# Kernel tuning notes

Measured on AMD Instinct MI355X. Metric: run time of the kernel, lower is better.

Reference implementation:

```python
import jax, jax.numpy as jnp
import numpy as np

NEG_SLOPE = 0.2
CHUNK = 64  # target-node chunk size to bound the [B,c,N,H,D] intermediate


def layer_norm(x, g, b, eps=1e-5):
    mu = jnp.mean(x, axis=-1, keepdims=True)
    var = jnp.mean((x - mu) ** 2, axis=-1, keepdims=True)
    return (x - mu) / jnp.sqrt(var + eps) * g + b


def gatv2_dense(x, Wl, bl, Wr, br, att, bias):
    """GATv2 (PyG semantics, concat=True) on a fully-connected graph with self-loops.
    x: [B,N,Fin]; att: [H,D]. Returns [B,N,H*D].
    e_ij = att_h . leaky_relu(xl_j + xr_i); softmax over sources j; out_i = sum_j a_ij xl_j.
    """
    B, N, _ = x.shape
    H, D = att.shape
    xl = (x @ Wl + bl).reshape(B, N, H, D)  # source-side (lin_l)
    xr = (x @ Wr + br).reshape(B, N, H, D)  # target-side (lin_r)
    nc = N // CHUNK
    xr_ch = jnp.moveaxis(xr.reshape(B, nc, CHUNK, H, D), 1, 0)  # [nc,B,c,H,D]

    @jax.checkpoint
    def per_chunk(xr_c):  # xr_c: [B,c,H,D]
        z = jax.nn.leaky_relu(xr_c[:, :, None] + xl[:, None], NEG_SLOPE)  # [B,c,N,H,D]
        e = jnp.einsum('bcjhd,hd->bcjh', z, att)
        a = jax.nn.softmax(e, axis=2)  # softmax over sources j
        return jnp.einsum('bcjh,bjhd->bchd', a, xl)

    out = jax.lax.map(per_chunk, xr_ch)  # [nc,B,c,H,D]
    return jnp.moveaxis(out, 0, 1).reshape(B, N, H * D) + bias


def setup_inputs() -> dict:
    key = jax.random.key(0)
    ks = jax.random.split(key, 12)
    B, N, Fin, Hd, H, Do = 4, 2048, 32, 32, 4, 32
    f32 = jnp.float32

    def glorot(k, shape, fan_in):
        return jax.random.normal(k, shape, f32) * (1.0 / np.sqrt(fan_in))

    return {
        'x': jax.random.normal(ks[0], (B, N, Fin), f32),
        'embedding': jax.random.normal(ks[1], (N, Hd), f32),
        # layer 1: in=Fin, heads=H, head dim=Hd
        'Wl1': glorot(ks[2], (Fin, H * Hd), Fin), 'bl1': jnp.zeros((H * Hd,), f32),
        'Wr1': glorot(ks[3], (Fin, H * Hd), Fin), 'br1': jnp.zeros((H * Hd,), f32),
        'att1': glorot(ks[4], (H, Hd), Hd), 'bias1': jnp.zeros((H * Hd,), f32),
        'ln1_g': jnp.ones((H * Hd,), f32), 'ln1_b': jnp.zeros((H * Hd,), f32),
        # layer 2: in=H*Hd, heads=H, head dim=Do
        'Wl2': glorot(ks[5], (H * Hd, H * Do), H * Hd), 'bl2': jnp.zeros((H * Do,), f32),
        'Wr2': glorot(ks[6], (H * Hd, H * Do), H * Hd), 'br2': jnp.zeros((H * Do,), f32),
        'att2': glorot(ks[7], (H, Do), Do), 'bias2': jnp.zeros((H * Do,), f32),
        'ln2_g': jnp.ones((H * Do,), f32), 'ln2_b': jnp.zeros((H * Do,), f32),
    }


def reference(x, embedding, Wl1, bl1, Wr1, br1, att1, bias1, ln1_g, ln1_b,
              Wl2, bl2, Wr2, br2, att2, bias2, ln2_g, ln2_b):
    # AdaptiveAdjacency: cosine-similarity gram matrix. Its values are generically
    # all nonzero, so adj[b].nonzero() yields a fully-connected edge list including
    # self-loops; only the connectivity (dense) is consumed downstream.
    ne = embedding / jnp.linalg.norm(embedding, axis=1, keepdims=True)
    adj = ne @ ne.T  # [N,N]; connectivity only (dense), values unused by GATv2
    del adj

    h = layer_norm(gatv2_dense(x, Wl1, bl1, Wr1, br1, att1, bias1), ln1_g, ln1_b)
    h = jax.nn.relu(h)
    # dropout(p=0.3) is identity in eval mode
    out = layer_norm(gatv2_dense(h, Wl2, bl2, Wr2, br2, att2, bias2), ln2_g, ln2_b)
    return out
```

## Files before the change

kernel.cpp:

```cpp
#include <hip/hip_runtime.h>
#include <math.h>

#define LOG2E 1.4426950408889634f

#if __has_builtin(__builtin_amdgcn_exp2f)
#define EXP2(x) __builtin_amdgcn_exp2f(x)
#else
#define EXP2(x) exp2f(x)
#endif

constexpr int B_ = 4, N_ = 2048, H_ = 4, D_ = 32, HD_ = 128;
constexpr int BH_ = B_ * H_;
constexpr int ROWS_ = BH_ * N_;
constexpr size_t M_ = (size_t)ROWS_ * D_;

typedef float v4f __attribute__((ext_vector_type(4)));
typedef _Float16 h2 __attribute__((ext_vector_type(2)));

static __device__ __forceinline__ h2 habs2(h2 z) {
    unsigned int t = __builtin_bit_cast(unsigned int, z) & 0x7FFF7FFFu;
    return __builtin_bit_cast(h2, t);
}
static __device__ __forceinline__ h2 hadd2u(unsigned int a, unsigned int b) {
    return __builtin_bit_cast(h2, a) + __builtin_bit_cast(h2, b);
}
static __device__ __forceinline__ h2 u2h(unsigned int a) {
    return __builtin_bit_cast(h2, a);
}

__global__ __launch_bounds__(256) void k_linear(
    const float* __restrict__ x,
    const float* __restrict__ Wl, const float* __restrict__ bl,
    const float* __restrict__ Wr, const float* __restrict__ br,
    float* __restrict__ xl, unsigned short* __restrict__ xlh,
    unsigned short* __restrict__ xrh, unsigned int* __restrict__ xlpT, int K)
{
    __shared__ __align__(16) float xs[32 * 128];
    const int tid = threadIdx.x;
    const int r0 = blockIdx.x * 32;
    const float4* src = (const float4*)(x + (size_t)r0 * K);
    float4* dst = (float4*)xs;
    for (int idx = tid; idx < 8 * K; idx += 256) dst[idx] = src[idx];
    __syncthreads();

    const int c  = tid & 127;
    const int rg = tid >> 7;
    float accl[16], accr[16];
    const float blv = bl[c], brv = br[c];
    #pragma unroll
    for (int r = 0; r < 16; r++) { accl[r] = blv; accr[r] = brv; }
    #pragma unroll 8
    for (int k = 0; k < K; k++) {
        const float wl = Wl[k * HD_ + c];
        const float wr = Wr[k * HD_ + c];
        #pragma unroll
        for (int r = 0; r < 16; r++) {
            const float xv = xs[(rg * 16 + r) * K + k];
            accl[r] = fmaf(xv, wl, accl[r]);
            accr[r] = fmaf(xv, wr, accr[r]);
        }
    }
    const int h = c >> 5, d = c & 31;
    #pragma unroll
    for (int r = 0; r < 16; r++) {
        const int row = r0 + rg * 16 + r;
        const int b = row >> 11, n = row & (N_ - 1);
        const size_t o = (((size_t)(b * H_ + h)) * N_ + n) * D_ + d;
        xl[o] = accl[r];
        xlh[o] = __builtin_bit_cast(unsigned short, (_Float16)accl[r]);
        xrh[o] = __builtin_bit_cast(unsigned short, (_Float16)accr[r]);
    }
    #pragma unroll
    for (int r = 0; r < 16; r += 2) {
        const int row = r0 + rg * 16 + r;
        const int b = row >> 11, n = row & (N_ - 1);
        h2 pr;
        pr.x = (_Float16)accl[r];
        pr.y = (_Float16)accl[r + 1];
        const size_t o = (((size_t)(b * H_ + h)) * (N_ / 2) + (n >> 1)) * D_ + d;
        xlpT[o] = __builtin_bit_cast(unsigned int, pr);
    }
}

__global__ __launch_bounds__(256) void k_u(
    const float* __restrict__ xl, const float* __restrict__ att,
    float* __restrict__ u)
{
    const int idx = blockIdx.x * 256 + threadIdx.x;
    const int h = (idx / N_) & (H_ - 1);
    const float4* a4 = (const float4*)(att + h * D_);
    const float4* l4 = (const float4*)(xl + (size_t)idx * D_);
    float su = 0.f;
    #pragma unroll
    for (int q = 0; q < 8; q++) {
        const float4 a = a4[q], lv = l4[q];
        su += a.x * lv.x + a.y * lv.y + a.z * lv.z + a.w * lv.w;
    }
    u[idx] = 0.6f * LOG2E * su;
}

__global__ __launch_bounds__(512) void k_bound(
    const unsigned int* __restrict__ xlh, const unsigned int* __restrict__ xrh,
    const float* __restrict__ u, const float* __restrict__ att,
    float* __restrict__ bound, unsigned int* __restrict__ tch)
{
    __shared__ float redA[16][33];
    __shared__ float redB[16][33];
    __shared__ float clv[32];
    __shared__ float tca[32];
    __shared__ float redu[512];
    const int bh = blockIdx.x, h = bh & (H_ - 1), t = threadIdx.x;

    if (bh < H_ && t < 16) {
        h2 v;
        v.x = (_Float16)(att[bh * D_ + 2 * t]     * (0.4f * LOG2E));
        v.y = (_Float16)(att[bh * D_ + 2 * t + 1] * (0.4f * LOG2E));
        tch[bh * 16 + t] = __builtin_bit_cast(unsigned int, v);
    }
    if (t < 16) {
        _Float16 a = (_Float16)(att[h * D_ + 2 * t]     * (0.4f * LOG2E));
        _Float16 b = (_Float16)(att[h * D_ + 2 * t + 1] * (0.4f * LOG2E));
        tca[2 * t]     = fabsf((float)a);
        tca[2 * t + 1] = fabsf((float)b);
    }
    const unsigned int* xb = xlh + (size_t)bh * N_ * 16;
    const int p = t & 15, rg = t >> 4;
    float m0 = 0.f, m1 = 0.f;
    for (int r = rg; r < N_; r += 32) {
        h2 z = __builtin_bit_cast(h2, xb[r * 16 + p] & 0x7FFF7FFFu);
        m0 = fmaxf(m0, (float)z.x);
        m1 = fmaxf(m1, (float)z.y);
    }
    redA[p][rg] = m0; redB[p][rg] = m1;
    const float* ub = u + (size_t)bh * N_;
    float um = -1e30f;
    for (int r = t; r < N_; r += 512) um = fmaxf(um, ub[r]);
    redu[t] = um;
    __syncthreads();
    if (t < 16) {
        float a = 0.f, b = 0.f;
        for (int g = 0; g < 32; g++) { a = fmaxf(a, redA[t][g]); b = fmaxf(b, redB[t][g]); }
        clv[2 * t] = a; clv[2 * t + 1] = b;
    }
    for (int s = 256; s > 0; s >>= 1) {
        if (t < s) redu[t] = fmaxf(redu[t], redu[t + s]);
        __syncthreads();
    }
    const float umax = redu[0];
    const unsigned int* xrb = xrh + (size_t)bh * N_ * 16;
    for (int r = t; r < N_; r += 512) {
        float s = 0.f;
        #pragma unroll
        for (int k = 0; k < 16; k++) {
            h2 z = __builtin_bit_cast(h2, xrb[r * 16 + k] & 0x7FFF7FFFu);
            s += tca[2 * k] * (clv[2 * k] + (float)z.x)
               + tca[2 * k + 1] * (clv[2 * k + 1] + (float)z.y);
        }
        bound[bh * N_ + r] = umax + s + 0.25f;
    }
}

__global__ __launch_bounds__(256)
__attribute__((amdgpu_waves_per_eu(3, 4)))
void k_attn(
    const unsigned int* __restrict__ xlh,
    const unsigned int* __restrict__ xlpT,
    const unsigned int* __restrict__ xrh,
    const float* __restrict__ u, const float* __restrict__ bound,
    const unsigned int* __restrict__ tch,
    float* __restrict__ P, float* __restrict__ lb, int jlen)
{
    const int tid = threadIdx.x, lane = tid & 63, wid = tid >> 6;
    const int t128 = blockIdx.x & 127, part = blockIdx.x >> 7;
    const int bh = t128 >> 3;
    const int h  = bh & (H_ - 1);
    const int row = bh * N_ + (t128 & 7) * 256 + wid * 64 + lane;

    unsigned int tcs[16];
    #pragma unroll
    for (int k = 0; k < 16; k++)
        tcs[k] = __builtin_amdgcn_readfirstlane(tch[h * 16 + k]);

    unsigned int xrp[16];
    {
        const uint4* s = (const uint4*)(xrh + (size_t)row * 16);
        const uint4 a = s[0], b = s[1], c = s[2], d = s[3];
        xrp[0]=a.x; xrp[1]=a.y; xrp[2]=a.z; xrp[3]=a.w;
        xrp[4]=b.x; xrp[5]=b.y; xrp[6]=b.z; xrp[7]=b.w;
        xrp[8]=c.x; xrp[9]=c.y; xrp[10]=c.z; xrp[11]=c.w;
        xrp[12]=d.x; xrp[13]=d.y; xrp[14]=d.z; xrp[15]=d.w;
    }
    const float negb = -bound[row];

    float l = 0.f;
    float o[32];
    #pragma unroll
    for (int k = 0; k < 32; k++) o[k] = 0.f;

    const unsigned int* xlh_b = xlh + (size_t)bh * N_ * 16;
    const unsigned int* xlt_b = xlpT + (size_t)bh * (N_ / 2) * 32;
    const float* u_b = u + (size_t)bh * N_;

    const int jpb = (part * jlen) >> 1, jpe = jpb + (jlen >> 1);
    for (int jp = jpb; jp < jpe; jp++) {
        const unsigned int* w0 = xlh_b + (size_t)(2 * jp) * 16;
        const unsigned int* w1 = w0 + 16;
        float e0 = u_b[2 * jp]     + negb;
        float f0 = 0.f, e1 = u_b[2 * jp + 1] + negb, f1 = 0.f;
        #pragma unroll
        for (int k = 0; k < 16; k += 2) {
            e0 = __builtin_amdgcn_fdot2(habs2(hadd2u(w0[k],     xrp[k])),     u2h(tcs[k]),     e0, false);
            f0 = __builtin_amdgcn_fdot2(habs2(hadd2u(w0[k + 1], xrp[k + 1])), u2h(tcs[k + 1]), f0, false);
            e1 = __builtin_amdgcn_fdot2(habs2(hadd2u(w1[k],     xrp[k])),     u2h(tcs[k]),     e1, false);
            f1 = __builtin_amdgcn_fdot2(habs2(hadd2u(w1[k + 1], xrp[k + 1])), u2h(tcs[k + 1]), f1, false);
        }
        const float p0 = EXP2(e0 + f0);
        const float p1 = EXP2(e1 + f1);
        const h2 p01 = __builtin_bit_cast(h2, __builtin_amdgcn_cvt_pkrtz(p0, p1));
        h2 ones; ones.x = (_Float16)1.f; ones.y = (_Float16)1.f;
        l = __builtin_amdgcn_fdot2(p01, ones, l, false);
        const unsigned int* vp = xlt_b + (size_t)jp * 32;
        #pragma unroll
        for (int d = 0; d < 32; d++)
            o[d] = __builtin_amdgcn_fdot2(p01, u2h(vp[d]), o[d], false);
    }

    float* Pp = P + (size_t)part * M_ + (size_t)row * D_;
    #pragma unroll
    for (int k = 0; k < 8; k++) {
        v4f w;
        w.x = o[4*k]; w.y = o[4*k+1]; w.z = o[4*k+2]; w.w = o[4*k+3];
        ((v4f*)Pp)[k] = w;
    }
    lb[part * ROWS_ + row] = l;
}

template <int JS>
__global__ __launch_bounds__(64) void k_comb_ln(
    const float* __restrict__ P, const float* __restrict__ lb,
    const float* __restrict__ bias, const float* __restrict__ g,
    const float* __restrict__ bta, float* __restrict__ outp, int do_relu)
{
    const int row = blockIdx.x;
    const int b = row >> 11, n = row & (N_ - 1);
    const int t = threadIdx.x;
    const int c0 = t, c1 = t + 64;
    const int bh0 = b * H_ + (c0 >> 5), bh1 = b * H_ + (c1 >> 5);
    const size_t i0 = ((size_t)bh0 * N_ + n) * D_ + (c0 & 31);
    const size_t i1 = ((size_t)bh1 * N_ + n) * D_ + (c1 & 31);
    float a0 = 0.f, a1 = 0.f, L0 = 0.f, L1 = 0.f;
    #pragma unroll
    for (int s = 0; s < JS; s++) {
        a0 += P[(size_t)s * M_ + i0];
        a1 += P[(size_t)s * M_ + i1];
        L0 += lb[s * ROWS_ + bh0 * N_ + n];
        L1 += lb[s * ROWS_ + bh1 * N_ + n];
    }
    const float x0 = a0 / L0 + bias[c0];
    const float x1 = a1 / L1 + bias[c1];
    float s = x0 + x1;
    #pragma unroll
    for (int w = 1; w < 64; w <<= 1) s += __shfl_xor(s, w);
    const float mu = s * (1.f / 128.f);
    const float d0 = x0 - mu, d1 = x1 - mu;
    float q = d0 * d0 + d1 * d1;
    #pragma unroll
    for (int w = 1; w < 64; w <<= 1) q += __shfl_xor(q, w);
    const float rstd = rsqrtf(q * (1.f / 128.f) + 1e-5f);
    float y0 = d0 * rstd * g[c0] + bta[c0];
    float y1 = d1 * rstd * g[c1] + bta[c1];
    if (do_relu) { y0 = fmaxf(y0, 0.f); y1 = fmaxf(y1, 0.f); }
    outp[(size_t)row * HD_ + c0] = y0;
    outp[(size_t)row * HD_ + c1] = y1;
}

extern "C" void kernel_launch(void* const* d_in, const int* in_sizes, int n_in,
                              void* d_out, int out_size, void* d_ws, size_t ws_size,
                              hipStream_t stream) {
    const float* x    = (const float*)d_in[0];
    const float* Wl1  = (const float*)d_in[2];
    const float* bl1  = (const float*)d_in[3];
    const float* Wr1  = (const float*)d_in[4];
    const float* br1  = (const float*)d_in[5];
    const float* att1 = (const float*)d_in[6];
    const float* bias1= (const float*)d_in[7];
    const float* ln1g = (const float*)d_in[8];
    const float* ln1b = (const float*)d_in[9];
    const float* Wl2  = (const float*)d_in[10];
    const float* bl2  = (const float*)d_in[11];
    const float* Wr2  = (const float*)d_in[12];
    const float* br2  = (const float*)d_in[13];
    const float* att2 = (const float*)d_in[14];
    const float* bias2= (const float*)d_in[15];
    const float* ln2g = (const float*)d_in[16];
    const float* ln2b = (const float*)d_in[17];

    float* ws = (float*)d_ws;
    float* xl = ws;
    unsigned short* xlh = (unsigned short*)(xl + M_);
    unsigned short* xrh = xlh + M_;
    unsigned int* xlpT = (unsigned int*)(xrh + M_);
    float* u     = xl + (size_t)(2.5 * M_);
    float* bound = u + ROWS_;
    unsigned int* tch = (unsigned int*)(bound + ROWS_);

    int js = 1;
    for (int cand = 8; cand >= 1; cand >>= 1) {
        const size_t need = ((size_t)(3.5 * M_) + 2 * ROWS_ + 64
                             + (size_t)cand * (M_ + ROWS_)) * sizeof(float);
        if (ws_size >= need) { js = cand; break; }
    }
    const int jlen = N_ / js;

    float* P  = (float*)(tch + 64);
    float* lb = P + (size_t)js * M_;
    float* h  = lb + (size_t)js * ROWS_;
    float* outf = (float*)d_out;

    const int BN = B_ * N_;
    k_linear<<<BN / 32, 256, 0, stream>>>(x, Wl1, bl1, Wr1, br1, xl, xlh, xrh, xlpT, 32);
    k_u<<<ROWS_ / 256, 256, 0, stream>>>(xl, att1, u);
    k_bound<<<BH_, 512, 0, stream>>>((const unsigned int*)xlh, (const unsigned int*)xrh,
                                     u, att1, bound, tch);
    k_attn<<<128 * js, 256, 0, stream>>>((const unsigned int*)xlh, xlpT,
                                         (const unsigned int*)xrh, u, bound, tch, P, lb, jlen);
    if      (js == 8) k_comb_ln<8><<<BN, 64, 0, stream>>>(P, lb, bias1, ln1g, ln1b, h, 1);
    else if (js == 4) k_comb_ln<4><<<BN, 64, 0, stream>>>(P, lb, bias1, ln1g, ln1b, h, 1);
    else if (js == 2) k_comb_ln<2><<<BN, 64, 0, stream>>>(P, lb, bias1, ln1g, ln1b, h, 1);
    else              k_comb_ln<1><<<BN, 64, 0, stream>>>(P, lb, bias1, ln1g, ln1b, h, 1);
    k_linear<<<BN / 32, 256, 0, stream>>>(h, Wl2, bl2, Wr2, br2, xl, xlh, xrh, xlpT, 128);
    k_u<<<ROWS_ / 256, 256, 0, stream>>>(xl, att2, u);
    k_bound<<<BH_, 512, 0, stream>>>((const unsigned int*)xlh, (const unsigned int*)xrh,
                                     u, att2, bound, tch);
    k_attn<<<128 * js, 256, 0, stream>>>((const unsigned int*)xlh, xlpT,
                                         (const unsigned int*)xrh, u, bound, tch, P, lb, jlen);
    if      (js == 8) k_comb_ln<8><<<BN, 64, 0, stream>>>(P, lb, bias2, ln2g, ln2b, outf, 0);
    else if (js == 4) k_comb_ln<4><<<BN, 64, 0, stream>>>(P, lb, bias2, ln2g, ln2b, outf, 0);
    else if (js == 2) k_comb_ln<2><<<BN, 64, 0, stream>>>(P, lb, bias2, ln2g, ln2b, outf, 0);
    else              k_comb_ln<1><<<BN, 64, 0, stream>>>(P, lb, bias2, ln2g, ln2b, outf, 0);
}
```

Measured before the change: 489.3 us.

## Switch attention to fp32 with LDS-tiled source rows instead of packed fp16 dot2

New measurement: 638.6 us. 1.31x slower.

```diff
diff --git a/kernel.cpp b/kernel.cpp
--- a/kernel.cpp
+++ b/kernel.cpp
@@ -14,26 +14,11 @@
 constexpr int ROWS_ = BH_ * N_;
 constexpr size_t M_ = (size_t)ROWS_ * D_;
 
-typedef float v4f __attribute__((ext_vector_type(4)));
-typedef _Float16 h2 __attribute__((ext_vector_type(2)));
-
-static __device__ __forceinline__ h2 habs2(h2 z) {
-    unsigned int t = __builtin_bit_cast(unsigned int, z) & 0x7FFF7FFFu;
-    return __builtin_bit_cast(h2, t);
-}
-static __device__ __forceinline__ h2 hadd2u(unsigned int a, unsigned int b) {
-    return __builtin_bit_cast(h2, a) + __builtin_bit_cast(h2, b);
-}
-static __device__ __forceinline__ h2 u2h(unsigned int a) {
-    return __builtin_bit_cast(h2, a);
-}
-
 __global__ __launch_bounds__(256) void k_linear(
     const float* __restrict__ x,
     const float* __restrict__ Wl, const float* __restrict__ bl,
     const float* __restrict__ Wr, const float* __restrict__ br,
-    float* __restrict__ xl, unsigned short* __restrict__ xlh,
-    unsigned short* __restrict__ xrh, unsigned int* __restrict__ xlpT, int K)
+    float* __restrict__ xl, float* __restrict__ xrf, int K)
 {
     __shared__ __align__(16) float xs[32 * 128];
     const int tid = threadIdx.x;
@@ -67,18 +52,7 @@
         const int b = row >> 11, n = row & (N_ - 1);
         const size_t o = (((size_t)(b * H_ + h)) * N_ + n) * D_ + d;
         xl[o] = accl[r];
-        xlh[o] = __builtin_bit_cast(unsigned short, (_Float16)accl[r]);
-        xrh[o] = __builtin_bit_cast(unsigned short, (_Float16)accr[r]);
-    }
-    #pragma unroll
-    for (int r = 0; r < 16; r += 2) {
-        const int row = r0 + rg * 16 + r;
-        const int b = row >> 11, n = row & (N_ - 1);
-        h2 pr;
-        pr.x = (_Float16)accl[r];
-        pr.y = (_Float16)accl[r + 1];
-        const size_t o = (((size_t)(b * H_ + h)) * (N_ / 2) + (n >> 1)) * D_ + d;
-        xlpT[o] = __builtin_bit_cast(unsigned int, pr);
+        xrf[o] = accr[r];
     }
 }
 
@@ -100,95 +74,91 @@
 }
 
 __global__ __launch_bounds__(512) void k_bound(
-    const unsigned int* __restrict__ xlh, const unsigned int* __restrict__ xrh,
+    const float* __restrict__ xl, const float* __restrict__ xrf,
     const float* __restrict__ u, const float* __restrict__ att,
-    float* __restrict__ bound, unsigned int* __restrict__ tch)
-{
-    __shared__ float redA[16][33];
-    __shared__ float redB[16][33];
+    float* __restrict__ bound)
+{
+    __shared__ float tca[32];
+    __shared__ float redA[32][17];
     __shared__ float clv[32];
-    __shared__ float tca[32];
     __shared__ float redu[512];
     const int bh = blockIdx.x, h = bh & (H_ - 1), t = threadIdx.x;
 
-    if (bh < H_ && t < 16) {
-        h2 v;
-        v.x = (_Float16)(att[bh * D_ + 2 * t]     * (0.4f * LOG2E));
-        v.y = (_Float16)(att[bh * D_ + 2 * t + 1] * (0.4f * LOG2E));
-        tch[bh * 16 + t] = __builtin_bit_cast(unsigned int, v);
-    }
-    if (t < 16) {
-        _Float16 a = (_Float16)(att[h * D_ + 2 * t]     * (0.4f * LOG2E));
-        _Float16 b = (_Float16)(att[h * D_ + 2 * t + 1] * (0.4f * LOG2E));
-        tca[2 * t]     = fabsf((float)a);
-        tca[2 * t + 1] = fabsf((float)b);
-    }
-    const unsigned int* xb = xlh + (size_t)bh * N_ * 16;
-    const int p = t & 15, rg = t >> 4;
-    float m0 = 0.f, m1 = 0.f;
-    for (int r = rg; r < N_; r += 32) {
-        h2 z = __builtin_bit_cast(h2, xb[r * 16 + p] & 0x7FFF7FFFu);
-        m0 = fmaxf(m0, (float)z.x);
-        m1 = fmaxf(m1, (float)z.y);
-    }
-    redA[p][rg] = m0; redB[p][rg] = m1;
+    if (t < 32) tca[t] = fabsf(0.4f * LOG2E * att[h * D_ + t]);
+
+    const float* xb = xl + (size_t)bh * N_ * D_;
+    const int p = t & 31, rg = t >> 5;
+    float m0 = 0.f;
+    for (int r = rg; r < N_; r += 16)
+        m0 = fmaxf(m0, fabsf(xb[r * D_ + p]));
+    redA[p][rg] = m0;
     const float* ub = u + (size_t)bh * N_;
     float um = -1e30f;
     for (int r = t; r < N_; r += 512) um = fmaxf(um, ub[r]);
     redu[t] = um;
     __syncthreads();
-    if (t < 16) {
-        float a = 0.f, b = 0.f;
-        for (int g = 0; g < 32; g++) { a = fmaxf(a, redA[t][g]); b = fmaxf(b, redB[t][g]); }
-        clv[2 * t] = a; clv[2 * t + 1] = b;
+    if (t < 32) {
+        float a = 0.f;
+        for (int g = 0; g < 16; g++) a = fmaxf(a, redA[t][g]);
+        clv[t] = a;
     }
     for (int s = 256; s > 0; s >>= 1) {
         if (t < s) redu[t] = fmaxf(redu[t], redu[t + s]);
         __syncthreads();
     }
     const float umax = redu[0];
-    const unsigned int* xrb = xrh + (size_t)bh * N_ * 16;
+    const float* xrb = xrf + (size_t)bh * N_ * D_;
     for (int r = t; r < N_; r += 512) {
         float s = 0.f;
         #pragma unroll
-        for (int k = 0; k < 16; k++) {
-            h2 z = __builtin_bit_cast(h2, xrb[r * 16 + k] & 0x7FFF7FFFu);
-            s += tca[2 * k] * (clv[2 * k] + (float)z.x)
-               + tca[2 * k + 1] * (clv[2 * k + 1] + (float)z.y);
-        }
+        for (int k = 0; k < 32; k++)
+            s = fmaf(tca[k], clv[k] + fabsf(xrb[r * D_ + k]), s);
         bound[bh * N_ + r] = umax + s + 0.25f;
     }
 }
 
-__global__ __launch_bounds__(256)
-__attribute__((amdgpu_waves_per_eu(3, 4)))
-void k_attn(
-    const unsigned int* __restrict__ xlh,
-    const unsigned int* __restrict__ xlpT,
-    const unsigned int* __restrict__ xrh,
+#define SCR(S, B)                                          \
+    e0 = fmaf(tcr[B + 0], fabsf(S.x + xr[B + 0]), e0);     \
+    e1 = fmaf(tcr[B + 1], fabsf(S.y + xr[B + 1]), e1);     \
+    e2 = fmaf(tcr[B + 2], fabsf(S.z + xr[B + 2]), e2);     \
+    e3 = fmaf(tcr[B + 3], fabsf(S.w + xr[B + 3]), e3);
+#define PVC(S, B)                                          \
+    o[B + 0] = fmaf(p, S.x, o[B + 0]);                     \
+    o[B + 1] = fmaf(p, S.y, o[B + 1]);                     \
+    o[B + 2] = fmaf(p, S.z, o[B + 2]);                     \
+    o[B + 3] = fmaf(p, S.w, o[B + 3]);
+
+__global__ __launch_bounds__(256) void k_attn(
+    const float* __restrict__ xlf, const float* __restrict__ xrf,
     const float* __restrict__ u, const float* __restrict__ bound,
-    const unsigned int* __restrict__ tch,
+    const float* __restrict__ att,
     float* __restrict__ P, float* __restrict__ lb, int jlen)
 {
-    const int tid = threadIdx.x, lane = tid & 63, wid = tid >> 6;
+    __shared__ __align__(16) float4 s_xf[2048];
+    __shared__ float s_u[256];
+    const int tid = threadIdx.x;
     const int t128 = blockIdx.x & 127, part = blockIdx.x >> 7;
     const int bh = t128 >> 3;
     const int h  = bh & (H_ - 1);
-    const int row = bh * N_ + (t128 & 7) * 256 + wid * 64 + lane;
-
-    unsigned int tcs[16];
-    #pragma unroll
-    for (int k = 0; k < 16; k++)
-        tcs[k] = __builtin_amdgcn_readfirstlane(tch[h * 16 + k]);
-
-    unsigned int xrp[16];
+    const int row = bh * N_ + (t128 & 7) * 256 + tid;
+
+    float tcr[32];
+    #pragma unroll
+    for (int d = 0; d < 32; d++)
+        tcr[d] = __builtin_bit_cast(float, __builtin_amdgcn_readfirstlane(
+            __builtin_bit_cast(unsigned int, 0.4f * LOG2E * att[h * D_ + d])));
+
+    float xr[32];
     {
-        const uint4* s = (const uint4*)(xrh + (size_t)row * 16);
-        const uint4 a = s[0], b = s[1], c = s[2], d = s[3];
-        xrp[0]=a.x; xrp[1]=a.y; xrp[2]=a.z; xrp[3]=a.w;
-        xrp[4]=b.x; xrp[5]=b.y; xrp[6]=b.z; xrp[7]=b.w;
-        xrp[8]=c.x; xrp[9]=c.y; xrp[10]=c.z; xrp[11]=c.w;
-        xrp[12]=d.x; xrp[13]=d.y; xrp[14]=d.z; xrp[15]=d.w;
+        const float4* s = (const float4*)(xrf + (size_t)row * D_);
+        #pragma unroll
+        for (int q = 0; q < 8; q++) {
+            const float4 v = s[q];
+            xr[4 * q]     = v.x;
+            xr[4 * q + 1] = v.y;
+            xr[4 * q + 2] = v.z;
+            xr[4 * q + 3] = v.w;
+        }
     }
     const float negb = -bound[row];
 
@@ -197,40 +167,40 @@
     #pragma unroll
     for (int k = 0; k < 32; k++) o[k] = 0.f;
 
-    const unsigned int* xlh_b = xlh + (size_t)bh * N_ * 16;
-    const unsigned int* xlt_b = xlpT + (size_t)bh * (N_ / 2) * 32;
+    const float4* gx = (const float4*)(xlf + (size_t)bh * N_ * D_);
     const float* u_b = u + (size_t)bh * N_;
 
-    const int jpb = (part * jlen) >> 1, jpe = jpb + (jlen >> 1);
-    for (int jp = jpb; jp < jpe; jp++) {
-        const unsigned int* w0 = xlh_b + (size_t)(2 * jp) * 16;
-        const unsigned int* w1 = w0 + 16;
-        float e0 = u_b[2 * jp]     + negb;
-        float f0 = 0.f, e1 = u_b[2 * jp + 1] + negb, f1 = 0.f;
+    const int jbeg = part * jlen;
+    for (int jt = 0; jt < jlen; jt += 256) {
+        if (jt) __syncthreads();
+        const int j0 = jbeg + jt;
         #pragma unroll
-        for (int k = 0; k < 16; k += 2) {
-            e0 = __builtin_amdgcn_fdot2(habs2(hadd2u(w0[k],     xrp[k])),     u2h(tcs[k]),     e0, false);
-            f0 = __builtin_amdgcn_fdot2(habs2(hadd2u(w0[k + 1], xrp[k + 1])), u2h(tcs[k + 1]), f0, false);
-            e1 = __builtin_amdgcn_fdot2(habs2(hadd2u(w1[k],     xrp[k])),     u2h(tcs[k]),     e1, false);
-            f1 = __builtin_amdgcn_fdot2(habs2(hadd2u(w1[k + 1], xrp[k + 1])), u2h(tcs[k + 1]), f1, false);
+        for (int k = 0; k < 8; k++)
+            s_xf[tid + 256 * k] = gx[(size_t)j0 * 8 + tid + 256 * k];
+        s_u[tid] = u_b[j0 + tid];
+        __syncthreads();
+
+        for (int j = 0; j < 256; j++) {
+            const float4 S0 = s_xf[8 * j + 0], S1 = s_xf[8 * j + 1];
+            const float4 S2 = s_xf[8 * j + 2], S3 = s_xf[8 * j + 3];
+            const float4 S4 = s_xf[8 * j + 4], S5 = s_xf[8 * j + 5];
+            const float4 S6 = s_xf[8 * j + 6], S7 = s_xf[8 * j + 7];
+            float e0 = s_u[j] + negb, e1 = 0.f, e2 = 0.f, e3 = 0.f;
+            SCR(S0, 0)  SCR(S1, 4)  SCR(S2, 8)  SCR(S3, 12)
+            SCR(S4, 16) SCR(S5, 20) SCR(S6, 24) SCR(S7, 28)
+            const float p = EXP2((e0 + e1) + (e2 + e3));
+            l += p;
+            PVC(S0, 0)  PVC(S1, 4)  PVC(S2, 8)  PVC(S3, 12)
+            PVC(S4, 16) PVC(S5, 20) PVC(S6, 24) PVC(S7, 28)
         }
-        const float p0 = EXP2(e0 + f0);
-        const float p1 = EXP2(e1 + f1);
-        const h2 p01 = __builtin_bit_cast(h2, __builtin_amdgcn_cvt_pkrtz(p0, p1));
-        h2 ones; ones.x = (_Float16)1.f; ones.y = (_Float16)1.f;
-        l = __builtin_amdgcn_fdot2(p01, ones, l, false);
-        const unsigned int* vp = xlt_b + (size_t)jp * 32;
-        #pragma unroll
-        for (int d = 0; d < 32; d++)
-            o[d] = __builtin_amdgcn_fdot2(p01, u2h(vp[d]), o[d], false);
     }
 
     float* Pp = P + (size_t)part * M_ + (size_t)row * D_;
     #pragma unroll
     for (int k = 0; k < 8; k++) {
-        v4f w;
+        float4 w;
         w.x = o[4*k]; w.y = o[4*k+1]; w.z = o[4*k+2]; w.w = o[4*k+3];
-        ((v4f*)Pp)[k] = w;
+        ((float4*)Pp)[k] = w;
     }
     lb[part * ROWS_ + row] = l;
 }
@@ -296,44 +266,37 @@
     const float* ln2b = (const float*)d_in[17];
 
     float* ws = (float*)d_ws;
-    float* xl = ws;
-    unsigned short* xlh = (unsigned short*)(xl + M_);
-    unsigned short* xrh = xlh + M_;
-    unsigned int* xlpT = (unsigned int*)(xrh + M_);
-    float* u     = xl + (size_t)(2.5 * M_);
+    float* xl  = ws;
+    float* xrf = xl + M_;
+    float* u     = xrf + M_;
     float* bound = u + ROWS_;
-    unsigned int* tch = (unsigned int*)(bound + ROWS_);
 
     int js = 1;
     for (int cand = 8; cand >= 1; cand >>= 1) {
-        const size_t need = ((size_t)(3.5 * M_) + 2 * ROWS_ + 64
+        const size_t need = ((size_t)3 * M_ + 2 * ROWS_
                              + (size_t)cand * (M_ + ROWS_)) * sizeof(float);
         if (ws_size >= need) { js = cand; break; }
     }
     const int jlen = N_ / js;
 
-    float* P  = (float*)(tch + 64);
+    float* P  = bound + ROWS_;
     float* lb = P + (size_t)js * M_;
     float* h  = lb + (size_t)js * ROWS_;
     float* outf = (float*)d_out;
 
     const int BN = B_ * N_;
-    k_linear<<<BN / 32, 256, 0, stream>>>(x, Wl1, bl1, Wr1, br1, xl, xlh, xrh, xlpT, 32);
+    k_linear<<<BN / 32, 256, 0, stream>>>(x, Wl1, bl1, Wr1, br1, xl, xrf, 32);
     k_u<<<ROWS_ / 256, 256, 0, stream>>>(xl, att1, u);
-    k_bound<<<BH_, 512, 0, stream>>>((const unsigned int*)xlh, (const unsigned int*)xrh,
-                                     u, att1, bound, tch);
-    k_attn<<<128 * js, 256, 0, stream>>>((const unsigned int*)xlh, xlpT,
-                                         (const unsigned int*)xrh, u, bound, tch, P, lb, jlen);
+    k_bound<<<BH_, 512, 0, stream>>>(xl, xrf, u, att1, bound);
+    k_attn<<<128 * js, 256, 0, stream>>>(xl, xrf, u, bound, att1, P, lb, jlen);
     if      (js == 8) k_comb_ln<8><<<BN, 64, 0, stream>>>(P, lb, bias1, ln1g, ln1b, h, 1);
     else if (js == 4) k_comb_ln<4><<<BN, 64, 0, stream>>>(P, lb, bias1, ln1g, ln1b, h, 1);
     else if (js == 2) k_comb_ln<2><<<BN, 64, 0, stream>>>(P, lb, bias1, ln1g, ln1b, h, 1);
     else              k_comb_ln<1><<<BN, 64, 0, stream>>>(P, lb, bias1, ln1g, ln1b, h, 1);
-    k_linear<<<BN / 32, 256, 0, stream>>>(h, Wl2, bl2, Wr2, br2, xl, xlh, xrh, xlpT, 128);
+    k_linear<<<BN / 32, 256, 0, stream>>>(h, Wl2, bl2, Wr2, br2, xl, xrf, 128);
     k_u<<<ROWS_ / 256, 256, 0, stream>>>(xl, att2, u);
-    k_bound<<<BH_, 512, 0, stream>>>((const unsigned int*)xlh, (const unsigned int*)xrh,
-                                     u, att2, bound, tch);
-    k_attn<<<128 * js, 256, 0, stream>>>((const unsigned int*)xlh, xlpT,
-                                         (const unsigned int*)xrh, u, bound, tch, P, lb, jlen);
+    k_bound<<<BH_, 512, 0, stream>>>(xl, xrf, u, att2, bound);
+    k_attn<<<128 * js, 256, 0, stream>>>(xl, xrf, u, bound, att2, P, lb, jlen);
     if      (js == 8) k_comb_ln<8><<<BN, 64, 0, stream>>>(P, lb, bias2, ln2g, ln2b, outf, 0);
     else if (js == 4) k_comb_ln<4><<<BN, 64, 0, stream>>>(P, lb, bias2, ln2g, ln2b, outf, 0);
     else if (js == 2) k_comb_ln<2><<<BN, 64, 0, stream>>>(P, lb, bias2, ln2g, ln2b, outf, 0);
```
